# Performance work log

Hardware: AMD Instinct MI355X
Metric: run time of the kernel (lower is better)

The kernel has to match this reference:

```python
import jax, jax.numpy as jnp
import numpy as np


def setup_inputs() -> dict:
    key = jax.random.key(0)
    k1, k2, k3 = jax.random.split(key, 3)
    B, E, S = 8, 2048, 2048
    x = jax.random.normal(k1, (B, E, S), dtype=jnp.float32)
    weight = jax.random.normal(k2, (1, S), dtype=jnp.float32)
    diag_weight = jax.random.normal(k3, (1, S), dtype=jnp.float32)
    bias = jnp.zeros((S,), dtype=jnp.float32)
    decay_value = jnp.ones((2, 1), dtype=jnp.float32)
    return {"x": x, "weight": weight, "diag_weight": diag_weight,
            "bias": bias, "decay_value": decay_value}


def _build_matrix(weight, diag_weight, decay_value):
    # Upper-triangular (strict) decay matrix M[i,j] = v[i] * d**(j-i) for j>i,
    # plus diagonal M[j,j] = v2[j].  d = clip(decay_value[1], 0.9, 1.0).
    v = weight.reshape(-1)       # (S,)
    v2 = diag_weight.reshape(-1)  # (S,)
    S = v.shape[0]
    idx = jnp.arange(S)
    diff = idx[None, :] - idx[:, None]          # j - i, shape (S, S)
    d = jnp.clip(decay_value[1, 0], 0.9, 1.0)   # scalar
    strict_upper = jnp.where(diff > 0, v[:, None] * d ** diff, jnp.zeros((), dtype=v.dtype))
    return strict_upper + jnp.diag(v2)          # (S, S)


def reference(x, weight, diag_weight, bias, decay_value):
    # x: (B, E, S); mixes along the sequence axis with the causal-decay matrix.
    M = _build_matrix(weight, diag_weight, decay_value)
    out = jnp.einsum('bes,st->bet', x, M) + bias  # bias broadcasts over last (seq) dim
    return out
```

## Files before the change

### kernel.cpp

```cpp
#include <hip/hip_runtime.h>


#define SEQ 2048
#define THREADS 256
#define PER_THREAD 8

__global__ __launch_bounds__(THREADS) void decay_scan_kernel(
    const float* __restrict__ x,
    const float* __restrict__ weight,
    const float* __restrict__ diag_weight,
    const float* __restrict__ bias,
    const float* __restrict__ decay,
    float* __restrict__ out)
{
    const int row  = blockIdx.x;
    const long base = (long)row * SEQ;
    const int tid  = threadIdx.x;
    const int lane = tid & 63;
    const int wv   = tid >> 6;

    float d = decay[1];
    d = fminf(fmaxf(d, 0.9f), 1.0f);
    const float d2 = d * d, d4 = d2 * d2, d8 = d4 * d4;

    const int off = tid * PER_THREAD;

    const float4 x0 = *(const float4*)(x + base + off);
    const float4 x1 = *(const float4*)(x + base + off + 4);
    const float4 v0 = *(const float4*)(weight + off);
    const float4 v1 = *(const float4*)(weight + off + 4);

    float xs[PER_THREAD] = {x0.x, x0.y, x0.z, x0.w, x1.x, x1.y, x1.z, x1.w};
    float vs[PER_THREAD] = {v0.x, v0.y, v0.z, v0.w, v1.x, v1.y, v1.z, v1.w};

    float lp[PER_THREAD];
    float c = 0.f;
    #pragma unroll
    for (int k = 0; k < PER_THREAD; ++k) {
        lp[k] = c;
        c = d * (c + xs[k] * vs[k]);
    }

    float s = c, p = d8;
    #pragma unroll
    for (int o = 1; o < 64; o <<= 1) {
        float s2 = __shfl_up(s, o, 64);
        float p2 = __shfl_up(p, o, 64);
        if (lane >= o) { s = fmaf(s2, p, s); p = p2 * p; }
    }
    float es = __shfl_up(s, 1, 64);
    float ep = __shfl_up(p, 1, 64);
    if (lane == 0) { es = 0.f; ep = 1.f; }

    __shared__ float ws[4], wp[4];
    if (lane == 63) { ws[wv] = s; wp[wv] = p; }
    __syncthreads();
    float cs = 0.f;
    #pragma unroll
    for (int w = 0; w < 3; ++w) {
        if (w < wv) cs = fmaf(cs, wp[w], ws[w]);
    }
    const float C = fmaf(cs, ep, es);

    const float4 w0 = *(const float4*)(diag_weight + off);
    const float4 w1 = *(const float4*)(diag_weight + off + 4);
    const float4 b0 = *(const float4*)(bias + off);
    const float4 b1 = *(const float4*)(bias + off + 4);
    float v2s[PER_THREAD] = {w0.x, w0.y, w0.z, w0.w, w1.x, w1.y, w1.z, w1.w};
    float bs[PER_THREAD]  = {b0.x, b0.y, b0.z, b0.w, b1.x, b1.y, b1.z, b1.w};

    float res[PER_THREAD];
    float dk = 1.f;
    #pragma unroll
    for (int k = 0; k < PER_THREAD; ++k) {
        res[k] = fmaf(xs[k], v2s[k], fmaf(C, dk, lp[k]) + bs[k]);
        dk *= d;
    }

    float4 r0 = make_float4(res[0], res[1], res[2], res[3]);
    float4 r1 = make_float4(res[4], res[5], res[6], res[7]);
    *(float4*)(out + base + off)     = r0;
    *(float4*)(out + base + off + 4) = r1;
}

extern "C" void kernel_launch(void* const* d_in, const int* in_sizes, int n_in,
                              void* d_out, int out_size, void* d_ws, size_t ws_size,
                              hipStream_t stream) {
    const float* x           = (const float*)d_in[0];
    const float* weight      = (const float*)d_in[1];
    const float* diag_weight = (const float*)d_in[2];
    const float* bias        = (const float*)d_in[3];
    const float* decay       = (const float*)d_in[4];
    float* out = (float*)d_out;

    const int rows = in_sizes[0] / SEQ;
    decay_scan_kernel<<<rows, THREADS, 0, stream>>>(
        x, weight, diag_weight, bias, decay, out);
}
```

Measured before the change: 239.5 us.

## Process one row per wavefront with 32 elements per lane, removing block sync

Each wavefront now scans a full sequence row, with 4 rows per block and 32 contiguous elements per lane. This removes the shared-memory cross-wave combine and __syncthreads, and folds the diag/bias terms into the first pass. The cost is strided per-lane float4 accesses, which coalesce worse, plus more registers per thread.

```diff
diff --git a/kernel.cpp b/kernel.cpp
--- a/kernel.cpp
+++ b/kernel.cpp
@@ -3,7 +3,8 @@
 
 #define SEQ 2048
 #define THREADS 256
-#define PER_THREAD 8
+#define ROWS_PER_BLOCK 4
+#define PER_LANE 32
 
 __global__ __launch_bounds__(THREADS) void decay_scan_kernel(
     const float* __restrict__ x,
@@ -13,74 +14,57 @@
     const float* __restrict__ decay,
     float* __restrict__ out)
 {
-    const int row  = blockIdx.x;
-    const long base = (long)row * SEQ;
-    const int tid  = threadIdx.x;
-    const int lane = tid & 63;
-    const int wv   = tid >> 6;
+    const int lane = threadIdx.x & 63;
+    const int wv   = threadIdx.x >> 6;
+    const long row  = (long)blockIdx.x * ROWS_PER_BLOCK + wv;
+    const long base = row * SEQ;
+    const int col0 = lane * PER_LANE;
 
-    float d = decay[1];
-    d = fminf(fmaxf(d, 0.9f), 1.0f);
-    const float d2 = d * d, d4 = d2 * d2, d8 = d4 * d4;
+    float d = fminf(fmaxf(decay[1], 0.9f), 1.0f);
+    const float d2 = d * d, d3 = d2 * d, d4 = d2 * d2;
+    const float d8 = d4 * d4, d16 = d8 * d8, d32 = d16 * d16;
 
-    const int off = tid * PER_THREAD;
-
-    const float4 x0 = *(const float4*)(x + base + off);
-    const float4 x1 = *(const float4*)(x + base + off + 4);
-    const float4 v0 = *(const float4*)(weight + off);
-    const float4 v1 = *(const float4*)(weight + off + 4);
-
-    float xs[PER_THREAD] = {x0.x, x0.y, x0.z, x0.w, x1.x, x1.y, x1.z, x1.w};
-    float vs[PER_THREAD] = {v0.x, v0.y, v0.z, v0.w, v1.x, v1.y, v1.z, v1.w};
-
-    float lp[PER_THREAD];
+    float rp[PER_LANE];
     float c = 0.f;
     #pragma unroll
-    for (int k = 0; k < PER_THREAD; ++k) {
-        lp[k] = c;
-        c = d * (c + xs[k] * vs[k]);
+    for (int j = 0; j < PER_LANE / 4; ++j) {
+        const float4 xv = *(const float4*)(x + base + col0 + j * 4);
+        const float4 vv = *(const float4*)(weight + col0 + j * 4);
+        const float4 gv = *(const float4*)(diag_weight + col0 + j * 4);
+        const float4 bv = *(const float4*)(bias + col0 + j * 4);
+        const float xa[4] = {xv.x, xv.y, xv.z, xv.w};
+        const float va[4] = {vv.x, vv.y, vv.z, vv.w};
+        const float ga[4] = {gv.x, gv.y, gv.z, gv.w};
+        const float ba[4] = {bv.x, bv.y, bv.z, bv.w};
+        #pragma unroll
+        for (int k = 0; k < 4; ++k) {
+            rp[j * 4 + k] = fmaf(xa[k], ga[k], c + ba[k]);
+            c = d * fmaf(xa[k], va[k], c);
+        }
     }
 
-    float s = c, p = d8;
+    float s = c, p = d32;
     #pragma unroll
     for (int o = 1; o < 64; o <<= 1) {
-        float s2 = __shfl_up(s, o, 64);
-        float p2 = __shfl_up(p, o, 64);
+        const float s2 = __shfl_up(s, o, 64);
+        const float p2 = __shfl_up(p, o, 64);
         if (lane >= o) { s = fmaf(s2, p, s); p = p2 * p; }
     }
-    float es = __shfl_up(s, 1, 64);
-    float ep = __shfl_up(p, 1, 64);
-    if (lane == 0) { es = 0.f; ep = 1.f; }
+    float C = __shfl_up(s, 1, 64);
+    if (lane == 0) C = 0.f;
 
-    __shared__ float ws[4], wp[4];
-    if (lane == 63) { ws[wv] = s; wp[wv] = p; }
-    __syncthreads();
-    float cs = 0.f;
+    float dkc = 1.f;
     #pragma unroll
-    for (int w = 0; w < 3; ++w) {
-        if (w < wv) cs = fmaf(cs, wp[w], ws[w]);
+    for (int j = 0; j < PER_LANE / 4; ++j) {
+        const float t = C * dkc;
+        float4 o4;
+        o4.x = t + rp[j * 4 + 0];
+        o4.y = fmaf(t, d,  rp[j * 4 + 1]);
+        o4.z = fmaf(t, d2, rp[j * 4 + 2]);
+        o4.w = fmaf(t, d3, rp[j * 4 + 3]);
+        *(float4*)(out + base + col0 + j * 4) = o4;
+        dkc *= d4;
     }
-    const float C = fmaf(cs, ep, es);
-
-    const float4 w0 = *(const float4*)(diag_weight + off);
-    const float4 w1 = *(const float4*)(diag_weight + off + 4);
-    const float4 b0 = *(const float4*)(bias + off);
-    const float4 b1 = *(const float4*)(bias + off + 4);
-    float v2s[PER_THREAD] = {w0.x, w0.y, w0.z, w0.w, w1.x, w1.y, w1.z, w1.w};
-    float bs[PER_THREAD]  = {b0.x, b0.y, b0.z, b0.w, b1.x, b1.y, b1.z, b1.w};
-
-    float res[PER_THREAD];
-    float dk = 1.f;
-    #pragma unroll
-    for (int k = 0; k < PER_THREAD; ++k) {
-        res[k] = fmaf(xs[k], v2s[k], fmaf(C, dk, lp[k]) + bs[k]);
-        dk *= d;
-    }
-
-    float4 r0 = make_float4(res[0], res[1], res[2], res[3]);
-    float4 r1 = make_float4(res[4], res[5], res[6], res[7]);
-    *(float4*)(out + base + off)     = r0;
-    *(float4*)(out + base + off + 4) = r1;
 }
 
 extern "C" void kernel_launch(void* const* d_in, const int* in_sizes, int n_in,
@@ -94,6 +78,6 @@
     float* out = (float*)d_out;
 
     const int rows = in_sizes[0] / SEQ;
-    decay_scan_kernel<<<rows, THREADS, 0, stream>>>(
+    decay_scan_kernel<<<rows / ROWS_PER_BLOCK, THREADS, 0, stream>>>(
         x, weight, diag_weight, bias, decay, out);
 }
```

New measurement: 302.2 us. 26.2% more time.
